# Kernel optimization log

Hardware: AMD Instinct MI355X
Metric: run time of the kernel (lower is better)

The kernel has to match this reference:

```python
import jax, jax.numpy as jnp
import numpy as np

N = 50000
E = 800000
D = 96      # in_ch == hidden_ch
C = 10      # out_ch
L = 3       # num_layers


def setup_inputs() -> dict:
    key = jax.random.key(0)
    ks = jax.random.split(key, 8)
    x = jax.random.normal(ks[0], (N, D), dtype=jnp.float32)
    edge_index = jax.random.randint(ks[1], (2, E), 0, N, dtype=jnp.int64)
    s = 1.0 / np.sqrt(D)
    # stacked per-layer MLP params: Linear(D->D), ReLU, Linear(D->D)
    W1 = jax.random.uniform(ks[2], (L, D, D), jnp.float32, -s, s)
    B1 = jax.random.uniform(ks[3], (L, D), jnp.float32, -s, s)
    W2 = jax.random.uniform(ks[4], (L, D, D), jnp.float32, -s, s)
    B2 = jax.random.uniform(ks[5], (L, D), jnp.float32, -s, s)
    Wc = jax.random.uniform(ks[6], (D, C), jnp.float32, -s, s)
    Bc = jax.random.uniform(ks[7], (C,), jnp.float32, -s, s)
    return {"x": x, "edge_index": edge_index, "W1": W1, "B1": B1,
            "W2": W2, "B2": B2, "Wc": Wc, "Bc": Bc}


def reference(x, edge_index, W1, B1, W2, B2, Wc, Bc):
    src, dst = edge_index[0], edge_index[1]
    h = x
    for l in range(L):
        # GIN aggregation: (1+eps)*h + sum_{j->i} h_j, eps=0
        agg = jax.ops.segment_sum(h[src], dst, num_segments=N) + h
        # 2-layer MLP
        z = jnp.maximum(agg @ W1[l] + B1[l], 0.0)
        z = z @ W2[l] + B2[l]
        # post-conv ReLU (dropout p=0.0 is identity)
        h = jnp.maximum(z, 0.0)
    return h @ Wc + Bc
```

## Files before the change

kernel.cpp:

```cpp
#include <hip/hip_runtime.h>


#define TPB 256
#define LDA 104
#define BS 64

typedef __attribute__((ext_vector_type(8))) short bfrag8;
typedef __attribute__((ext_vector_type(8))) unsigned short u16x8;
typedef __attribute__((ext_vector_type(4))) float f32x4;

__device__ inline unsigned short f2bf(float x) {
  unsigned int u = __float_as_uint(x);
  unsigned int r = u + 0x7FFFu + ((u >> 16) & 1u);
  return (unsigned short)(r >> 16);
}
__device__ inline float bf2f(unsigned short u) {
  return __uint_as_float(((unsigned int)u) << 16);
}

__global__ __launch_bounds__(TPB) void prep_kernel(
    int* __restrict__ cursor, int N,
    const float* __restrict__ W1, const float* __restrict__ W2,
    unsigned short* __restrict__ wt,
    const float4* __restrict__ x4, u16x8* __restrict__ h8, int total8) {
  int t = blockIdx.x * TPB + threadIdx.x;
  if (t < N) { cursor[t] = 0; return; }
  t -= N;
  const int wjobs = 6 * 9216;
  if (t < wjobs) {
    int mat = t / 9216, idx = t - mat * 9216;
    int l = mat >> 1, which = mat & 1;
    int k = idx / 96, n = idx - k * 96;
    const float* src = (which ? W2 : W1) + (size_t)l * 9216;
    wt[(size_t)mat * 9216 + n * 96 + k] = f2bf(src[k * 96 + n]);
  } else {
    int u = t - wjobs;
    if (u < total8) {
      float4 a = x4[2 * u], b = x4[2 * u + 1];
      u16x8 o;
      o[0] = f2bf(a.x); o[1] = f2bf(a.y); o[2] = f2bf(a.z); o[3] = f2bf(a.w);
      o[4] = f2bf(b.x); o[5] = f2bf(b.y); o[6] = f2bf(b.z); o[7] = f2bf(b.w);
      h8[u] = o;
    }
  }
}

__global__ __launch_bounds__(TPB) void fill_kernel(const int* __restrict__ src,
                                                   const int* __restrict__ dst,
                                                   int* __restrict__ cursor,
                                                   unsigned short* __restrict__ csr16,
                                                   int N, int E) {
  const int g = blockIdx.x & 7;
  const int bid = blockIdx.x >> 3;
  const int nblk = gridDim.x >> 3;
  const int chunk = (N + 7) >> 3;
  const int lo = g * chunk;
  const unsigned span = (unsigned)((N - lo < chunk) ? (N - lo) : chunk);
  const int gsz = nblk * TPB;
  for (int t = bid * TPB + threadIdx.x; 4 * t < E; t += gsz) {
    int base = 4 * t;
    if (base + 4 <= E) {
      int4 d4 = *reinterpret_cast<const int4*>(dst + base);
      int4 s4 = *reinterpret_cast<const int4*>(src + base);
      if ((unsigned)(d4.x - lo) < span) {
        int slot = atomicAdd(&cursor[d4.x], 1);
        csr16[(size_t)d4.x * BS + slot] = (unsigned short)s4.x;
      }
      if ((unsigned)(d4.y - lo) < span) {
        int slot = atomicAdd(&cursor[d4.y], 1);
        csr16[(size_t)d4.y * BS + slot] = (unsigned short)s4.y;
      }
      if ((unsigned)(d4.z - lo) < span) {
        int slot = atomicAdd(&cursor[d4.z], 1);
        csr16[(size_t)d4.z * BS + slot] = (unsigned short)s4.z;
      }
      if ((unsigned)(d4.w - lo) < span) {
        int slot = atomicAdd(&cursor[d4.w], 1);
        csr16[(size_t)d4.w * BS + slot] = (unsigned short)s4.w;
      }
    } else {
      for (int e = base; e < E; e++) {
        int d = dst[e];
        if ((unsigned)(d - lo) < span) {
          int slot = atomicAdd(&cursor[d], 1);
          csr16[(size_t)d * BS + slot] = (unsigned short)src[e];
        }
      }
    }
  }
}

__global__ __launch_bounds__(TPB) void aggb_kernel(const u16x8* __restrict__ hin8,
                                                   u16x8* __restrict__ hout8,
                                                   const int* __restrict__ deg,
                                                   const unsigned short* __restrict__ csr16,
                                                   int n) {
  int t = blockIdx.x * TPB + threadIdx.x;
  if (t >= n * 12) return;
  int i = t / 12;
  int f = t - i * 12;
  const unsigned short* row = csr16 + (size_t)i * BS;
  u16x8 self = hin8[t];
  float acc[8];
#pragma unroll
  for (int k = 0; k < 8; k++) acc[k] = bf2f(self[k]);
  int e = deg[i];
  int j = 0;
  for (; j + 8 <= e; j += 8) {
    u16x8 idx = *reinterpret_cast<const u16x8*>(row + j);
    u16x8 v0 = hin8[(size_t)idx[0] * 12 + f];
    u16x8 v1 = hin8[(size_t)idx[1] * 12 + f];
    u16x8 v2 = hin8[(size_t)idx[2] * 12 + f];
    u16x8 v3 = hin8[(size_t)idx[3] * 12 + f];
    u16x8 v4 = hin8[(size_t)idx[4] * 12 + f];
    u16x8 v5 = hin8[(size_t)idx[5] * 12 + f];
    u16x8 v6 = hin8[(size_t)idx[6] * 12 + f];
    u16x8 v7 = hin8[(size_t)idx[7] * 12 + f];
#pragma unroll
    for (int k = 0; k < 8; k++)
      acc[k] += ((bf2f(v0[k]) + bf2f(v1[k])) + (bf2f(v2[k]) + bf2f(v3[k]))) +
                ((bf2f(v4[k]) + bf2f(v5[k])) + (bf2f(v6[k]) + bf2f(v7[k])));
  }
  if (j + 4 <= e) {
    int i0 = row[j], i1 = row[j + 1], i2 = row[j + 2], i3 = row[j + 3];
    u16x8 v0 = hin8[(size_t)i0 * 12 + f];
    u16x8 v1 = hin8[(size_t)i1 * 12 + f];
    u16x8 v2 = hin8[(size_t)i2 * 12 + f];
    u16x8 v3 = hin8[(size_t)i3 * 12 + f];
#pragma unroll
    for (int k = 0; k < 8; k++)
      acc[k] += (bf2f(v0[k]) + bf2f(v1[k])) + (bf2f(v2[k]) + bf2f(v3[k]));
    j += 4;
  }
  for (; j < e; j++) {
    u16x8 v = hin8[(size_t)row[j] * 12 + f];
#pragma unroll
    for (int k = 0; k < 8; k++) acc[k] += bf2f(v[k]);
  }
  u16x8 o;
#pragma unroll
  for (int k = 0; k < 8; k++) o[k] = f2bf(acc[k]);
  hout8[t] = o;
}

template <bool LAST>
__global__ __launch_bounds__(TPB) void mlp_mfma_kernel(
    const u16x8* __restrict__ in8, const unsigned short* __restrict__ wt1,
    const unsigned short* __restrict__ wt2, const float* __restrict__ B1,
    const float* __restrict__ B2, unsigned short* __restrict__ out,
    const float* __restrict__ Wc, const float* __restrict__ Bc,
    float* __restrict__ outf, int nrows) {
  __shared__ unsigned short A_lds[64 * LDA];
  __shared__ unsigned short W1_lds[96 * LDA];
  __shared__ unsigned short W2_lds[96 * LDA];
  const int tid = threadIdx.x;
  const int row0 = blockIdx.x * 64;

  for (int t = tid; t < 64 * 12; t += TPB) {
    int r = t / 12, c8 = t - r * 12;
    int gr = row0 + r;
    u16x8 v = {};
    if (gr < nrows) v = in8[(size_t)gr * 12 + c8];
    *reinterpret_cast<u16x8*>(&A_lds[r * LDA + 8 * c8]) = v;
  }
  for (int t = tid; t < 2 * 1152; t += TPB) {
    int which = t / 1152, idx = t - which * 1152;
    int n = idx / 12, c8 = idx - n * 12;
    const unsigned short* src = (which ? wt2 : wt1) + n * 96 + 8 * c8;
    bfrag8 v = *reinterpret_cast<const bfrag8*>(src);
    unsigned short* dp = (which ? W2_lds : W1_lds) + n * LDA + 8 * c8;
    *reinterpret_cast<bfrag8*>(dp) = v;
  }
  __syncthreads();

  const int lane = tid & 63;
  const int w = tid >> 6;
  const int nl = lane & 15;
  const int q = lane >> 4;
  const int arow = 16 * w + nl;

  bfrag8 afrag[3];
#pragma unroll
  for (int s = 0; s < 3; s++)
    afrag[s] = *reinterpret_cast<const bfrag8*>(&A_lds[arow * LDA + 32 * s + 8 * q]);

#pragma unroll
  for (int cb = 0; cb < 6; cb++) {
    f32x4 acc = {0.f, 0.f, 0.f, 0.f};
#pragma unroll
    for (int s = 0; s < 3; s++) {
      bfrag8 bfr = *reinterpret_cast<const bfrag8*>(
          &W1_lds[(16 * cb + nl) * LDA + 32 * s + 8 * q]);
      acc = __builtin_amdgcn_mfma_f32_16x16x32_bf16(afrag[s], bfr, acc, 0, 0, 0);
    }
    float b = B1[16 * cb + nl];
#pragma unroll
    for (int i = 0; i < 4; i++) {
      int m = 16 * w + 4 * q + i;
      A_lds[m * LDA + 16 * cb + nl] = f2bf(fmaxf(acc[i] + b, 0.f));
    }
  }

  bfrag8 zfrag[3];
#pragma unroll
  for (int s = 0; s < 3; s++)
    zfrag[s] = *reinterpret_cast<const bfrag8*>(&A_lds[arow * LDA + 32 * s + 8 * q]);

  float oacc[40];
#pragma unroll
  for (int t2 = 0; t2 < 40; t2++) oacc[t2] = 0.f;

#pragma unroll
  for (int cb = 0; cb < 6; cb++) {
    f32x4 acc = {0.f, 0.f, 0.f, 0.f};
#pragma unroll
    for (int s = 0; s < 3; s++) {
      bfrag8 bfr = *reinterpret_cast<const bfrag8*>(
          &W2_lds[(16 * cb + nl) * LDA + 32 * s + 8 * q]);
      acc = __builtin_amdgcn_mfma_f32_16x16x32_bf16(zfrag[s], bfr, acc, 0, 0, 0);
    }
    float b = B2[16 * cb + nl];
#pragma unroll
    for (int i = 0; i < 4; i++) {
      float hv = fmaxf(acc[i] + b, 0.f);
      if (!LAST) {
        int m = 16 * w + 4 * q + i;
        int gr = row0 + m;
        if (gr < nrows) out[(size_t)gr * 96 + 16 * cb + nl] = f2bf(hv);
      } else {
#pragma unroll
        for (int c = 0; c < 10; c++)
          oacc[i * 10 + c] += hv * Wc[(16 * cb + nl) * 10 + c];
      }
    }
  }

  if (LAST) {
#pragma unroll
    for (int m = 1; m < 16; m <<= 1) {
#pragma unroll
      for (int t2 = 0; t2 < 40; t2++) oacc[t2] += __shfl_xor(oacc[t2], m, 64);
    }
#pragma unroll
    for (int i = 0; i < 4; i++) {
      int gr = row0 + 16 * w + 4 * q + i;
      if (gr < nrows && nl < 10) {
        float v = 0.f;
#pragma unroll
        for (int c = 0; c < 10; c++)
          if (nl == c) v = oacc[i * 10 + c];
        outf[(size_t)gr * 10 + nl] = v + Bc[nl];
      }
    }
  }
}

extern "C" void kernel_launch(void* const* d_in, const int* in_sizes, int n_in,
                              void* d_out, int out_size, void* d_ws, size_t ws_size,
                              hipStream_t stream) {
  const float* x  = (const float*)d_in[0];
  const int*   ei = (const int*)d_in[1];
  const float* W1 = (const float*)d_in[2];
  const float* B1 = (const float*)d_in[3];
  const float* W2 = (const float*)d_in[4];
  const float* B2 = (const float*)d_in[5];
  const float* Wc = (const float*)d_in[6];
  const float* Bc = (const float*)d_in[7];
  float* out = (float*)d_out;

  const int N = in_sizes[0] / 96;
  const int E = in_sizes[1] / 2;
  const int* src = ei;
  const int* dst = ei + E;

  unsigned short* hbuf   = (unsigned short*)d_ws;
  unsigned short* aggbuf = hbuf + (size_t)N * 96;
  int* cursor = (int*)(aggbuf + (size_t)N * 96);
  unsigned short* csr16 = (unsigned short*)(cursor + N);
  unsigned short* wt    = csr16 + (size_t)N * BS;

  const int total8 = N * 12;
  const int prep_jobs = N + 6 * 9216 + total8;
  prep_kernel<<<(prep_jobs + TPB - 1) / TPB, TPB, 0, stream>>>(
      cursor, N, W1, W2, wt, (const float4*)x, (u16x8*)hbuf, total8);

  fill_kernel<<<1024, TPB, 0, stream>>>(src, dst, cursor, csr16, N, E);

  for (int l = 0; l < 3; l++) {
    aggb_kernel<<<((N * 12) + TPB - 1) / TPB, TPB, 0, stream>>>(
        (const u16x8*)hbuf, (u16x8*)aggbuf, cursor, csr16, N);
    const unsigned short* wt1 = wt + (size_t)(l * 2) * 9216;
    const unsigned short* wt2 = wt + (size_t)(l * 2 + 1) * 9216;
    const float* b1 = B1 + (size_t)l * 96;
    const float* b2 = B2 + (size_t)l * 96;
    if (l < 2)
      mlp_mfma_kernel<false><<<(N + 63) / 64, TPB, 0, stream>>>(
          (const u16x8*)aggbuf, wt1, wt2, b1, b2, hbuf, Wc, Bc, out, N);
    else
      mlp_mfma_kernel<true><<<(N + 63) / 64, TPB, 0, stream>>>(
          (const u16x8*)aggbuf, wt1, wt2, b1, b2, hbuf, Wc, Bc, out, N);
  }
}
```

Before: 189.2 us.

## Split node features into two column halves and aggregate each half separately

Stores the bf16 node feature matrix as two separate 48-column arrays and runs the gather-sum aggregation twice per layer, once per half. The aim is to shrink the gathered working set per pass (about 4.8 MB per half) so it fits better in L2/MALL cache and random neighbor gathers hit more often. The cost is an extra kernel launch per layer and reading the CSR index lists twice.

New measurement: 202.1 us. 6.8% more time.

```diff
diff --git a/kernel.cpp b/kernel.cpp
--- a/kernel.cpp
+++ b/kernel.cpp
@@ -22,7 +22,8 @@
     int* __restrict__ cursor, int N,
     const float* __restrict__ W1, const float* __restrict__ W2,
     unsigned short* __restrict__ wt,
-    const float4* __restrict__ x4, u16x8* __restrict__ h8, int total8) {
+    const float4* __restrict__ x4, unsigned short* __restrict__ hlo,
+    unsigned short* __restrict__ hhi, int total8) {
   int t = blockIdx.x * TPB + threadIdx.x;
   if (t < N) { cursor[t] = 0; return; }
   t -= N;
@@ -36,11 +37,14 @@
   } else {
     int u = t - wjobs;
     if (u < total8) {
+      int i = u / 12, c8 = u - i * 12;
       float4 a = x4[2 * u], b = x4[2 * u + 1];
       u16x8 o;
       o[0] = f2bf(a.x); o[1] = f2bf(a.y); o[2] = f2bf(a.z); o[3] = f2bf(a.w);
       o[4] = f2bf(b.x); o[5] = f2bf(b.y); o[6] = f2bf(b.z); o[7] = f2bf(b.w);
-      h8[u] = o;
+      unsigned short* dst = (c8 < 6) ? (hlo + (size_t)i * 48 + c8 * 8)
+                                     : (hhi + (size_t)i * 48 + (c8 - 6) * 8);
+      *reinterpret_cast<u16x8*>(dst) = o;
     }
   }
 }
@@ -90,17 +94,17 @@
   }
 }
 
-__global__ __launch_bounds__(TPB) void aggb_kernel(const u16x8* __restrict__ hin8,
-                                                   u16x8* __restrict__ hout8,
+__global__ __launch_bounds__(TPB) void aggb_kernel(const u16x8* __restrict__ hin6,
+                                                   u16x8* __restrict__ aggbuf12,
                                                    const int* __restrict__ deg,
                                                    const unsigned short* __restrict__ csr16,
-                                                   int n) {
+                                                   int n, int half) {
   int t = blockIdx.x * TPB + threadIdx.x;
-  if (t >= n * 12) return;
-  int i = t / 12;
-  int f = t - i * 12;
+  if (t >= n * 6) return;
+  int i = t / 6;
+  int f = t - i * 6;
   const unsigned short* row = csr16 + (size_t)i * BS;
-  u16x8 self = hin8[t];
+  u16x8 self = hin6[(size_t)i * 6 + f];
   float acc[8];
 #pragma unroll
   for (int k = 0; k < 8; k++) acc[k] = bf2f(self[k]);
@@ -108,14 +112,14 @@
   int j = 0;
   for (; j + 8 <= e; j += 8) {
     u16x8 idx = *reinterpret_cast<const u16x8*>(row + j);
-    u16x8 v0 = hin8[(size_t)idx[0] * 12 + f];
-    u16x8 v1 = hin8[(size_t)idx[1] * 12 + f];
-    u16x8 v2 = hin8[(size_t)idx[2] * 12 + f];
-    u16x8 v3 = hin8[(size_t)idx[3] * 12 + f];
-    u16x8 v4 = hin8[(size_t)idx[4] * 12 + f];
-    u16x8 v5 = hin8[(size_t)idx[5] * 12 + f];
-    u16x8 v6 = hin8[(size_t)idx[6] * 12 + f];
-    u16x8 v7 = hin8[(size_t)idx[7] * 12 + f];
+    u16x8 v0 = hin6[(size_t)idx[0] * 6 + f];
+    u16x8 v1 = hin6[(size_t)idx[1] * 6 + f];
+    u16x8 v2 = hin6[(size_t)idx[2] * 6 + f];
+    u16x8 v3 = hin6[(size_t)idx[3] * 6 + f];
+    u16x8 v4 = hin6[(size_t)idx[4] * 6 + f];
+    u16x8 v5 = hin6[(size_t)idx[5] * 6 + f];
+    u16x8 v6 = hin6[(size_t)idx[6] * 6 + f];
+    u16x8 v7 = hin6[(size_t)idx[7] * 6 + f];
 #pragma unroll
     for (int k = 0; k < 8; k++)
       acc[k] += ((bf2f(v0[k]) + bf2f(v1[k])) + (bf2f(v2[k]) + bf2f(v3[k]))) +
@@ -123,31 +127,32 @@
   }
   if (j + 4 <= e) {
     int i0 = row[j], i1 = row[j + 1], i2 = row[j + 2], i3 = row[j + 3];
-    u16x8 v0 = hin8[(size_t)i0 * 12 + f];
-    u16x8 v1 = hin8[(size_t)i1 * 12 + f];
-    u16x8 v2 = hin8[(size_t)i2 * 12 + f];
-    u16x8 v3 = hin8[(size_t)i3 * 12 + f];
+    u16x8 v0 = hin6[(size_t)i0 * 6 + f];
+    u16x8 v1 = hin6[(size_t)i1 * 6 + f];
+    u16x8 v2 = hin6[(size_t)i2 * 6 + f];
+    u16x8 v3 = hin6[(size_t)i3 * 6 + f];
 #pragma unroll
     for (int k = 0; k < 8; k++)
       acc[k] += (bf2f(v0[k]) + bf2f(v1[k])) + (bf2f(v2[k]) + bf2f(v3[k]));
     j += 4;
   }
   for (; j < e; j++) {
-    u16x8 v = hin8[(size_t)row[j] * 12 + f];
+    u16x8 v = hin6[(size_t)row[j] * 6 + f];
 #pragma unroll
     for (int k = 0; k < 8; k++) acc[k] += bf2f(v[k]);
   }
   u16x8 o;
 #pragma unroll
   for (int k = 0; k < 8; k++) o[k] = f2bf(acc[k]);
-  hout8[t] = o;
+  aggbuf12[(size_t)i * 12 + 6 * half + f] = o;
 }
 
 template <bool LAST>
 __global__ __launch_bounds__(TPB) void mlp_mfma_kernel(
     const u16x8* __restrict__ in8, const unsigned short* __restrict__ wt1,
     const unsigned short* __restrict__ wt2, const float* __restrict__ B1,
-    const float* __restrict__ B2, unsigned short* __restrict__ out,
+    const float* __restrict__ B2, unsigned short* __restrict__ hlo,
+    unsigned short* __restrict__ hhi,
     const float* __restrict__ Wc, const float* __restrict__ Bc,
     float* __restrict__ outf, int nrows) {
   __shared__ unsigned short A_lds[64 * LDA];
@@ -226,7 +231,11 @@
       if (!LAST) {
         int m = 16 * w + 4 * q + i;
         int gr = row0 + m;
-        if (gr < nrows) out[(size_t)gr * 96 + 16 * cb + nl] = f2bf(hv);
+        if (gr < nrows) {
+          int col = 16 * cb + nl;
+          if (cb < 3) hlo[(size_t)gr * 48 + col] = f2bf(hv);
+          else        hhi[(size_t)gr * 48 + (col - 48)] = f2bf(hv);
+        }
       } else {
 #pragma unroll
         for (int c = 0; c < 10; c++)
@@ -273,8 +282,9 @@
   const int* src = ei;
   const int* dst = ei + E;
 
-  unsigned short* hbuf   = (unsigned short*)d_ws;
-  unsigned short* aggbuf = hbuf + (size_t)N * 96;
+  unsigned short* hlo    = (unsigned short*)d_ws;
+  unsigned short* hhi    = hlo + (size_t)N * 48;
+  unsigned short* aggbuf = hhi + (size_t)N * 48;
   int* cursor = (int*)(aggbuf + (size_t)N * 96);
   unsigned short* csr16 = (unsigned short*)(cursor + N);
   unsigned short* wt    = csr16 + (size_t)N * BS;
@@ -282,22 +292,25 @@
   const int total8 = N * 12;
   const int prep_jobs = N + 6 * 9216 + total8;
   prep_kernel<<<(prep_jobs + TPB - 1) / TPB, TPB, 0, stream>>>(
-      cursor, N, W1, W2, wt, (const float4*)x, (u16x8*)hbuf, total8);
+      cursor, N, W1, W2, wt, (const float4*)x, hlo, hhi, total8);
 
   fill_kernel<<<1024, TPB, 0, stream>>>(src, dst, cursor, csr16, N, E);
 
+  const int aggblk = (N * 6 + TPB - 1) / TPB;
   for (int l = 0; l < 3; l++) {
-    aggb_kernel<<<((N * 12) + TPB - 1) / TPB, TPB, 0, stream>>>(
-        (const u16x8*)hbuf, (u16x8*)aggbuf, cursor, csr16, N);
+    aggb_kernel<<<aggblk, TPB, 0, stream>>>(
+        (const u16x8*)hlo, (u16x8*)aggbuf, cursor, csr16, N, 0);
+    aggb_kernel<<<aggblk, TPB, 0, stream>>>(
+        (const u16x8*)hhi, (u16x8*)aggbuf, cursor, csr16, N, 1);
     const unsigned short* wt1 = wt + (size_t)(l * 2) * 9216;
     const unsigned short* wt2 = wt + (size_t)(l * 2 + 1) * 9216;
     const float* b1 = B1 + (size_t)l * 96;
     const float* b2 = B2 + (size_t)l * 96;
     if (l < 2)
       mlp_mfma_kernel<false><<<(N + 63) / 64, TPB, 0, stream>>>(
-          (const u16x8*)aggbuf, wt1, wt2, b1, b2, hbuf, Wc, Bc, out, N);
+          (const u16x8*)aggbuf, wt1, wt2, b1, b2, hlo, hhi, Wc, Bc, out, N);
     else
       mlp_mfma_kernel<true><<<(N + 63) / 64, TPB, 0, stream>>>(
-          (const u16x8*)aggbuf, wt1, wt2, b1, b2, hbuf, Wc, Bc, out, N);
-  }
-}
+          (const u16x8*)aggbuf, wt1, wt2, b1, b2, hlo, hhi, Wc, Bc, out, N);
+  }
+}
```
